# Kernel tuning notes

Hardware: AMD Instinct MI355X
Metric: run time of the kernel (lower is better)

## Reference

```python
import jax, jax.numpy as jnp
import numpy as np

D = 512
H = 8
DH = D // H
EPS = 1e-5


def layer_norm(x, gamma, beta):
    mu = jnp.mean(x, axis=-1, keepdims=True)
    var = jnp.mean(jnp.square(x - mu), axis=-1, keepdims=True)
    return (x - mu) * jax.lax.rsqrt(var + EPS) * gamma + beta


def setup_inputs() -> dict:
    key = jax.random.key(0)
    ks = jax.random.split(key, 16)
    B, N = 16, 1024
    s = 1.0 / np.sqrt(D)
    return {
        "h": jax.random.normal(ks[0], (B, N, D), jnp.float32),
        "ln1_g": jnp.ones((D,), jnp.float32),
        "ln1_b": jnp.zeros((D,), jnp.float32),
        "wq": jax.random.normal(ks[1], (D, D), jnp.float32) * s,
        "bq": jnp.zeros((D,), jnp.float32),
        "wk": jax.random.normal(ks[2], (D, D), jnp.float32) * s,
        "bk": jnp.zeros((D,), jnp.float32),
        "wv": jax.random.normal(ks[3], (D, D), jnp.float32) * s,
        "bv": jnp.zeros((D,), jnp.float32),
        "wo": jax.random.normal(ks[4], (D, D), jnp.float32) * s,
        "bo": jnp.zeros((D,), jnp.float32),
        "ln2_g": jnp.ones((D,), jnp.float32),
        "ln2_b": jnp.zeros((D,), jnp.float32),
        "w1": jax.random.normal(ks[5], (2 * D, D), jnp.float32) * s,
        "b1": jnp.zeros((2 * D,), jnp.float32),
        "w2": jax.random.normal(ks[6], (D, 2 * D), jnp.float32) * (1.0 / np.sqrt(2 * D)),
        "b2": jnp.zeros((D,), jnp.float32),
    }


def reference(h, ln1_g, ln1_b, wq, bq, wk, bk, wv, bv, wo, bo,
              ln2_g, ln2_b, w1, b1, w2, b2):
    B, N, _ = h.shape
    hn = layer_norm(h, ln1_g, ln1_b)
    # projections (torch Linear convention: x @ W^T + b)
    q = (hn @ wq.T + bq).reshape(B, N, H, DH)
    k = (hn @ wk.T + bk).reshape(B, N, H, DH)
    v = (hn @ wv.T + bv).reshape(B, N, H, DH)
    scores = jnp.einsum("bqhd,bkhd->bhqk", q, k) / np.sqrt(DH)
    attn = jax.nn.softmax(scores, axis=-1)  # [B,H,N,N]
    ctx = jnp.einsum("bhqk,bkhd->bqhd", attn, v).reshape(B, N, D)
    attn_out = ctx @ wo.T + bo
    # averaged attention weights (torch default average_attn_weights=True)
    attn_weights = jnp.mean(attn, axis=1)  # [B,N,N]
    h = h + attn_out
    # FFN: LN -> Linear(d,2d) -> SiLU -> Linear(2d,d), residual
    f = layer_norm(h, ln2_g, ln2_b)
    f = jax.nn.silu(f @ w1.T + b1) @ w2.T + b2
    h = h + f
    return h, attn_weights
```

## Files before the change

### kernel.cpp

```cpp
#include <hip/hip_runtime.h>

typedef unsigned short u16;
typedef __attribute__((ext_vector_type(8))) short short8;
typedef __attribute__((ext_vector_type(4))) float floatx4;
typedef __attribute__((ext_vector_type(16))) float floatx16;

#define MFMA_BF16(a, b, c) __builtin_amdgcn_mfma_f32_16x16x32_bf16((a), (b), (c), 0, 0, 0)
#define MFMA32(a, b, c) __builtin_amdgcn_mfma_f32_32x32x16_bf16((a), (b), (c), 0, 0, 0)

__device__ __forceinline__ u16 f2bf(float f) {
  unsigned b = __float_as_uint(f);
  b = b + 0x7FFFu + ((b >> 16) & 1u);
  return (u16)(b >> 16);
}

__device__ __forceinline__ float fexp8(float s) {
  float r;
  asm("v_exp_f32 %0, %1" : "=v"(r) : "v"(s * 0.18033688011112042f));
  return r;
}

__device__ __forceinline__ unsigned cvtpk(float a, float b) {
  unsigned r;
  asm("v_cvt_pk_bf16_f32 %0, %1, %2" : "=v"(r) : "v"(a), "v"(b));
  return r;
}

__device__ __forceinline__ void plswap(unsigned& x, unsigned& y) {
  asm("v_permlane32_swap_b32 %0, %1" : "+v"(x), "+v"(y));
}

__device__ __forceinline__ void gll16(const u16* g, u16* lds_uniform) {
  __builtin_amdgcn_global_load_lds(
      (const __attribute__((address_space(1))) void*)g,
      (__attribute__((address_space(3))) void*)lds_uniform, 16, 0, 0);
}

__global__ __launch_bounds__(256) void cast4_kernel(const float* __restrict__ src,
                                                    u16* __restrict__ dst, int n4) {
  int i = blockIdx.x * 256 + threadIdx.x;
  if (i < n4) {
    float4 v = ((const float4*)src)[i];
    ushort4 o;
    o.x = f2bf(v.x); o.y = f2bf(v.y); o.z = f2bf(v.z); o.w = f2bf(v.w);
    ((ushort4*)dst)[i] = o;
  }
}

__global__ __launch_bounds__(128) void ln_kernel(const float* __restrict__ x,
                                                 const float* __restrict__ g,
                                                 const float* __restrict__ be,
                                                 u16* __restrict__ y) {
  int row = blockIdx.x, t = threadIdx.x;
  float4 v = ((const float4*)(x + (size_t)row * 512))[t];
  float s = v.x + v.y + v.z + v.w;
  float q = v.x * v.x + v.y * v.y + v.z * v.z + v.w * v.w;
#pragma unroll
  for (int off = 32; off > 0; off >>= 1) {
    s += __shfl_xor(s, off);
    q += __shfl_xor(q, off);
  }
  __shared__ float sb[2], qb[2];
  int w = t >> 6;
  if ((t & 63) == 0) { sb[w] = s; qb[w] = q; }
  __syncthreads();
  s = sb[0] + sb[1];
  q = qb[0] + qb[1];
  float mu = s * (1.0f / 512.0f);
  float var = q * (1.0f / 512.0f) - mu * mu;
  float rs = rsqrtf(var + 1e-5f);
  float4 gg = ((const float4*)g)[t];
  float4 bb = ((const float4*)be)[t];
  ushort4 o;
  o.x = f2bf((v.x - mu) * rs * gg.x + bb.x);
  o.y = f2bf((v.y - mu) * rs * gg.y + bb.y);
  o.z = f2bf((v.z - mu) * rs * gg.z + bb.z);
  o.w = f2bf((v.w - mu) * rs * gg.w + bb.w);
  ((ushort4*)(y + (size_t)row * 512))[t] = o;
}

template <bool OUTB, bool SILU, bool RES>
__global__ __launch_bounds__(256) void gemm_bt_kernel(
    const u16* __restrict__ A, const u16* __restrict__ W,
    const float* __restrict__ bias, const float* __restrict__ res,
    void* __restrict__ out, int N, int K) {
  __shared__ __align__(16) u16 As[128 * 32];
  __shared__ __align__(16) u16 Bs[128 * 32];
  int t = threadIdx.x;
  int lane = t & 63, wave = t >> 6;
  int l15 = lane & 15, quad = lane >> 4;
  int rowBlk = blockIdx.y * 128, colBlk = blockIdx.x * 128;
  const u16* Ag = A + (size_t)(rowBlk + (t >> 2)) * K + (t & 3) * 8;
  const u16* Wg = W + (size_t)(colBlk + (t >> 2)) * K + (t & 3) * 8;
  u16* AsW = As + wave * 512;
  u16* BsW = Bs + wave * 512;
  int arow = (wave >> 1) * 64;
  int brow = (wave & 1) * 64;
  floatx4 acc[4][4] = {};
  for (int k0 = 0; k0 < K; k0 += 32) {
    gll16(Ag + k0, AsW);
    gll16(Ag + (size_t)64 * K + k0, AsW + 2048);
    gll16(Wg + k0, BsW);
    gll16(Wg + (size_t)64 * K + k0, BsW + 2048);
    __syncthreads();
    short8 a[4], b[4];
#pragma unroll
    for (int i = 0; i < 4; ++i)
      a[i] = *(const short8*)(As + (size_t)(arow + i * 16 + l15) * 32 + quad * 8);
#pragma unroll
    for (int j = 0; j < 4; ++j)
      b[j] = *(const short8*)(Bs + (size_t)(brow + j * 16 + l15) * 32 + quad * 8);
#pragma unroll
    for (int i = 0; i < 4; ++i)
#pragma unroll
      for (int j = 0; j < 4; ++j)
        acc[i][j] = MFMA_BF16(a[i], b[j], acc[i][j]);
    __syncthreads();
  }
#pragma unroll
  for (int j = 0; j < 4; ++j) {
    int col = colBlk + brow + j * 16 + l15;
    float bs = bias[col];
#pragma unroll
    for (int i = 0; i < 4; ++i) {
      int row0 = rowBlk + arow + i * 16 + quad * 4;
#pragma unroll
      for (int r = 0; r < 4; ++r) {
        size_t idx = (size_t)(row0 + r) * N + col;
        float v = acc[i][j][r] + bs;
        if (RES) v += res[idx];
        if (SILU) v = v * (1.0f / (1.0f + __expf(-v)));
        if (OUTB) ((u16*)out)[idx] = f2bf(v);
        else ((float*)out)[idx] = v;
      }
    }
  }
}

__global__ __launch_bounds__(256) void vtrans_kernel(const u16* __restrict__ qkv,
                                                     u16* __restrict__ vT) {
  __shared__ u16 tile[64][68];
  int blk = blockIdx.x;
  int b = blk >> 7, h = (blk >> 4) & 7, n0 = (blk & 15) * 64;
  int t = threadIdx.x;
#pragma unroll
  for (int rep = 0; rep < 16; ++rep) {
    int idx = t + rep * 256;
    int nl = idx >> 6, dh = idx & 63;
    tile[nl][dh] = qkv[(size_t)(b * 1024 + n0 + nl) * 1536 + 1024 + h * 64 + dh];
  }
  __syncthreads();
#pragma unroll
  for (int rep = 0; rep < 16; ++rep) {
    int idx = t + rep * 256;
    int dh = idx >> 6, nl = idx & 63;
    vT[((size_t)(b * 8 + h) * 64 + dh) * 1024 + n0 + nl] = tile[nl][dh];
  }
}

__global__ __launch_bounds__(256, 4) void attn_ctx_kernel(const u16* __restrict__ qkv,
                                                          const u16* __restrict__ vT,
                                                          u16* __restrict__ ctx,
                                                          float* __restrict__ linv_g) {
  __shared__ __align__(16) u16 Kb[2][4096];
  __shared__ __align__(16) u16 Vb[2][4096];
  int t = threadIdx.x, lane = t & 63, wave = t >> 6;
  int l31 = lane & 31, hi = lane >> 5;
  int bid = blockIdx.x;
  int L = (bid & 7) * 128 + (bid >> 3);
  int qblk = L & 7, h = (L >> 3) & 7, b = L >> 6;
  int q0w = qblk * 128 + wave * 32;

  short8 qf[4];
  const u16* qbase = qkv + (size_t)(b * 1024 + q0w + l31) * 1536 + h * 64;
#pragma unroll
  for (int t4 = 0; t4 < 4; ++t4)
    qf[t4] = *(const short8*)(qbase + t4 * 16 + hi * 8);

  short8 ones;
#pragma unroll
  for (int i = 0; i < 8; ++i) ones[i] = (short)0x3F80;

  floatx16 oacc[2] = {};
  floatx16 psum = {};

  const u16* krow = qkv + (size_t)(b * 1024 + lane) * 1536 + 512 + h * 64;
  const u16* vrow = vT + ((size_t)(b * 8 + h) * 64 + lane) * 1024;

  gll16(krow + wave * 8, &Kb[0][wave * 512]);
  gll16(krow + (wave + 4) * 8, &Kb[0][(wave + 4) * 512]);
  gll16(vrow + wave * 8, &Vb[0][wave * 512]);
  gll16(vrow + (wave + 4) * 8, &Vb[0][(wave + 4) * 512]);
  __syncthreads();

#pragma unroll 1
  for (int c = 0; c < 16; ++c) {
    int bf = c & 1;
    if (c < 15) {
      int nc = (c + 1) * 64;
      gll16(krow + (size_t)nc * 1536 + wave * 8, &Kb[bf ^ 1][wave * 512]);
      gll16(krow + (size_t)nc * 1536 + (wave + 4) * 8, &Kb[bf ^ 1][(wave + 4) * 512]);
      gll16(vrow + nc + wave * 8, &Vb[bf ^ 1][wave * 512]);
      gll16(vrow + nc + (wave + 4) * 8, &Vb[bf ^ 1][(wave + 4) * 512]);
    }
    short8 pa[4];
#pragma unroll
    for (int ct = 0; ct < 2; ++ct) {
      floatx16 s = {};
#pragma unroll
      for (int t4 = 0; t4 < 4; ++t4) {
        short8 kf = *(const short8*)&Kb[bf][(t4 * 2 + hi) * 512 + (ct * 32 + l31) * 8];
        s = MFMA32(kf, qf[t4], s);
      }
#pragma unroll
      for (int r = 0; r < 16; ++r) s[r] = fexp8(s[r]);
#pragma unroll
      for (int j = 0; j < 2; ++j) {
        unsigned a0 = cvtpk(s[j * 8 + 0], s[j * 8 + 1]);
        unsigned b0 = cvtpk(s[j * 8 + 4], s[j * 8 + 5]);
        unsigned a1 = cvtpk(s[j * 8 + 2], s[j * 8 + 3]);
        unsigned b1 = cvtpk(s[j * 8 + 6], s[j * 8 + 7]);
        plswap(a0, b0);
        plswap(a1, b1);
        union { unsigned u[4]; short8 v8; } uu;
        uu.u[0] = a0; uu.u[1] = a1; uu.u[2] = b0; uu.u[3] = b1;
        pa[ct * 2 + j] = uu.v8;
      }
    }
#pragma unroll
    for (int ks = 0; ks < 4; ++ks) {
      psum = MFMA32(pa[ks], ones, psum);
#pragma unroll
      for (int ct2 = 0; ct2 < 2; ++ct2) {
        short8 vf = *(const short8*)&Vb[bf][(ks * 2 + hi) * 512 + (ct2 * 32 + l31) * 8];
        oacc[ct2] = MFMA32(pa[ks], vf, oacc[ct2]);
      }
    }
    __syncthreads();
  }

  float il[16];
#pragma unroll
  for (int r = 0; r < 16; ++r) il[r] = 1.0f / psum[r];
  if (l31 == 0) {
#pragma unroll
    for (int reg = 0; reg < 16; ++reg) {
      int row = (reg & 3) + 8 * (reg >> 2) + 4 * hi;
      linv_g[(size_t)(b * 8 + h) * 1024 + q0w + row] = il[reg];
    }
  }
#pragma unroll
  for (int ct = 0; ct < 2; ++ct)
#pragma unroll
    for (int reg = 0; reg < 16; ++reg) {
      int row = (reg & 3) + 8 * (reg >> 2) + 4 * hi;
      ctx[(size_t)(b * 1024 + q0w + row) * 512 + h * 64 + ct * 32 + l31] =
          f2bf(oacc[ct][reg] * il[reg]);
    }
}

__global__ __launch_bounds__(256, 2) void attn_avg_kernel(const u16* __restrict__ qkv,
                                                          const float* __restrict__ linv_g,
                                                          float* __restrict__ attnw) {
  __shared__ __align__(16) u16 Ks[8 * 4096];
  int t = threadIdx.x, lane = t & 63, wave = t >> 6;
  int l31 = lane & 31, hi = lane >> 5;
  int bid = blockIdx.x;
  int L = (bid & 7) * 64 + (bid >> 3);
  int b = L >> 5;
  int r5 = L & 31;
  int kq = r5 & 3, qb = r5 >> 2;
  int q0w = qb * 128 + wave * 32;
  int key0 = kq * 256;

  const u16* qbase = qkv + (size_t)(b * 1024 + q0w + l31) * 1536;

  floatx16 avgacc[2] = {};
#pragma unroll 1
  for (int c = 0; c < 4; ++c) {
    const u16* kbase = qkv + (size_t)(b * 1024 + key0 + c * 64 + lane) * 1536 + 512;
#pragma unroll
    for (int s = 0; s < 16; ++s) {
      int idx = wave * 16 + s;
      int hh = idx >> 3, g = idx & 7;
      gll16(kbase + hh * 64 + g * 8, Ks + hh * 4096 + g * 512);
    }
    __syncthreads();
#pragma unroll 2
    for (int h = 0; h < 8; ++h) {
      short8 qf[4];
#pragma unroll
      for (int t4 = 0; t4 < 4; ++t4)
        qf[t4] = *(const short8*)(qbase + h * 64 + t4 * 16 + hi * 8);
      const float* lg = linv_g + (size_t)(b * 8 + h) * 1024 + q0w + 4 * hi;
      float4 il0 = *(const float4*)(lg);
      float4 il1 = *(const float4*)(lg + 8);
      float4 il2 = *(const float4*)(lg + 16);
      float4 il3 = *(const float4*)(lg + 24);
      float il[16] = {il0.x, il0.y, il0.z, il0.w, il1.x, il1.y, il1.z, il1.w,
                      il2.x, il2.y, il2.z, il2.w, il3.x, il3.y, il3.z, il3.w};
#pragma unroll
      for (int ct = 0; ct < 2; ++ct) {
        floatx16 sacc = {};
#pragma unroll
        for (int t4 = 0; t4 < 4; ++t4) {
          short8 kf = *(const short8*)(Ks + h * 4096 + (t4 * 2 + hi) * 512 +
                                       (ct * 32 + l31) * 8);
          sacc = MFMA32(qf[t4], kf, sacc);
        }
#pragma unroll
        for (int r = 0; r < 16; ++r)
          avgacc[ct][r] += fexp8(sacc[r]) * il[r];
      }
    }
    __syncthreads();
    int cb = key0 + c * 64;
#pragma unroll
    for (int ct = 0; ct < 2; ++ct)
#pragma unroll
      for (int r = 0; r < 16; ++r) {
        int row = (r & 3) + 8 * (r >> 2) + 4 * hi;
        __builtin_nontemporal_store(
            avgacc[ct][r] * 0.125f,
            &attnw[(size_t)(b * 1024 + q0w + row) * 1024 + cb + ct * 32 + l31]);
        avgacc[ct][r] = 0.f;
      }
  }
}

extern "C" void kernel_launch(void* const* d_in, const int* in_sizes, int n_in,
                              void* d_out, int out_size, void* d_ws, size_t ws_size,
                              hipStream_t stream) {
  (void)in_sizes; (void)n_in; (void)out_size; (void)ws_size;
  const float* h   = (const float*)d_in[0];
  const float* g1  = (const float*)d_in[1];
  const float* be1 = (const float*)d_in[2];
  const float* wq  = (const float*)d_in[3];
  const float* bq  = (const float*)d_in[4];
  const float* wk  = (const float*)d_in[5];
  const float* bk  = (const float*)d_in[6];
  const float* wv  = (const float*)d_in[7];
  const float* bv  = (const float*)d_in[8];
  const float* wo  = (const float*)d_in[9];
  const float* bo  = (const float*)d_in[10];
  const float* g2  = (const float*)d_in[11];
  const float* be2 = (const float*)d_in[12];
  const float* w1  = (const float*)d_in[13];
  const float* b1  = (const float*)d_in[14];
  const float* w2  = (const float*)d_in[15];
  const float* b2  = (const float*)d_in[16];

  char* p = (char*)d_ws;
  auto carve = [&](size_t bytes) {
    char* r = p;
    p += (bytes + 255) & ~(size_t)255;
    return r;
  };
  u16*   wcat = (u16*)carve((size_t)1536 * 512 * 2);
  u16*   wob  = (u16*)carve((size_t)512 * 512 * 2);
  u16*   w1b  = (u16*)carve((size_t)1024 * 512 * 2);
  u16*   w2b  = (u16*)carve((size_t)512 * 1024 * 2);
  float* bcat = (float*)carve((size_t)1536 * 4);
  u16*   hn   = (u16*)carve((size_t)16384 * 512 * 2);
  u16*   qkvb = (u16*)carve((size_t)16384 * 1536 * 2);
  u16*   vTb  = (u16*)carve((size_t)16384 * 512 * 2);
  u16*   ctxb = (u16*)carve((size_t)16384 * 512 * 2);
  u16*   fb   = (u16*)carve((size_t)16384 * 512 * 2);
  u16*   gb   = (u16*)carve((size_t)16384 * 1024 * 2);
  float* linv = (float*)carve((size_t)16 * 8 * 1024 * 4);

  float* outh = (float*)d_out;
  float* outattn = outh + (size_t)16384 * 512;

  cast4_kernel<<<256, 256, 0, stream>>>(wq, wcat, 65536);
  cast4_kernel<<<256, 256, 0, stream>>>(wk, wcat + 512 * 512, 65536);
  cast4_kernel<<<256, 256, 0, stream>>>(wv, wcat + 2 * 512 * 512, 65536);
  cast4_kernel<<<256, 256, 0, stream>>>(wo, wob, 65536);
  cast4_kernel<<<512, 256, 0, stream>>>(w1, w1b, 131072);
  cast4_kernel<<<512, 256, 0, stream>>>(w2, w2b, 131072);
  hipMemcpyAsync(bcat, bq, 512 * 4, hipMemcpyDeviceToDevice, stream);
  hipMemcpyAsync(bcat + 512, bk, 512 * 4, hipMemcpyDeviceToDevice, stream);
  hipMemcpyAsync(bcat + 1024, bv, 512 * 4, hipMemcpyDeviceToDevice, stream);

  ln_kernel<<<16384, 128, 0, stream>>>(h, g1, be1, hn);
  gemm_bt_kernel<true, false, false><<<dim3(12, 128), 256, 0, stream>>>(
      hn, wcat, bcat, nullptr, qkvb, 1536, 512);
  vtrans_kernel<<<2048, 256, 0, stream>>>(qkvb, vTb);
  attn_ctx_kernel<<<1024, 256, 0, stream>>>(qkvb, vTb, ctxb, linv);
  attn_avg_kernel<<<512, 256, 0, stream>>>(qkvb, linv, outattn);
  gemm_bt_kernel<false, false, true><<<dim3(4, 128), 256, 0, stream>>>(
      ctxb, wob, bo, h, outh, 512, 512);
  ln_kernel<<<16384, 128, 0, stream>>>(outh, g2, be2, fb);
  gemm_bt_kernel<true, true, false><<<dim3(8, 128), 256, 0, stream>>>(
      fb, w1b, b1, nullptr, gb, 1024, 512);
  gemm_bt_kernel<false, false, true><<<dim3(4, 128), 256, 0, stream>>>(
      gb, w2b, b2, outh, outh, 512, 1024);
}
```

Baseline: 438.2 us.

## Restructure attention-average kernel: smaller key tiles, staged swizzled Q/K in LDS

The attention-weight averaging kernel now gives each block 64 keys instead of 256 and launches four times as many blocks. Each block loops over heads and stages both Q and K per head into XOR-swizzled LDS tiles, instead of loading Q from global per head with a large 64KB K buffer. LDS use drops from 64KB to 24KB, and launch bounds rise to 4 blocks per SM to improve occupancy and reduce bank conflicts. In exchange, each Q tile is reloaded by 16 blocks instead of 4, which adds global and L2 traffic, and the kernel now syncs once per head.

```diff
diff --git a/kernel.cpp b/kernel.cpp
--- a/kernel.cpp
+++ b/kernel.cpp
@@ -259,72 +259,88 @@
     }
 }
 
-__global__ __launch_bounds__(256, 2) void attn_avg_kernel(const u16* __restrict__ qkv,
+__global__ __launch_bounds__(256, 4) void attn_avg_kernel(const u16* __restrict__ qkv,
                                                           const float* __restrict__ linv_g,
                                                           float* __restrict__ attnw) {
-  __shared__ __align__(16) u16 Ks[8 * 4096];
+  __shared__ __align__(16) u16 Qs[128 * 64];
+  __shared__ __align__(16) u16 Ks[64 * 64];
   int t = threadIdx.x, lane = t & 63, wave = t >> 6;
   int l31 = lane & 31, hi = lane >> 5;
   int bid = blockIdx.x;
-  int L = (bid & 7) * 64 + (bid >> 3);
-  int b = L >> 5;
-  int r5 = L & 31;
-  int kq = r5 & 3, qb = r5 >> 2;
-  int q0w = qb * 128 + wave * 32;
-  int key0 = kq * 256;
-
-  const u16* qbase = qkv + (size_t)(b * 1024 + q0w + l31) * 1536;
-
-  floatx16 avgacc[2] = {};
+  int L = (bid & 7) * 256 + (bid >> 3);
+  int b = L >> 7;
+  int r7 = L & 127;
+  int kq = r7 & 15, qb = r7 >> 4;
+  int q0 = qb * 128;
+  int q0w = q0 + wave * 32;
+  int key0 = kq * 64;
+
+  int li = lane >> 3, sl = lane & 7;
+
+  floatx16 acc0 = {}, acc1 = {};
+
 #pragma unroll 1
-  for (int c = 0; c < 4; ++c) {
-    const u16* kbase = qkv + (size_t)(b * 1024 + key0 + c * 64 + lane) * 1536 + 512;
-#pragma unroll
-    for (int s = 0; s < 16; ++s) {
-      int idx = wave * 16 + s;
-      int hh = idx >> 3, g = idx & 7;
-      gll16(kbase + hh * 64 + g * 8, Ks + hh * 4096 + g * 512);
+  for (int h = 0; h < 8; ++h) {
+    {
+      const u16* qsec = qkv + (size_t)(b * 1024 + q0) * 1536 + h * 64;
+#pragma unroll
+      for (int j = 0; j < 4; ++j) {
+        int r0 = wave * 32 + j * 8;
+        int row = r0 + li;
+        gll16(qsec + (size_t)row * 1536 + ((sl ^ (row & 7)) << 3), Qs + r0 * 64);
+      }
+      const u16* ksec = qkv + (size_t)(b * 1024 + key0) * 1536 + 512 + h * 64;
+#pragma unroll
+      for (int j = 0; j < 2; ++j) {
+        int r0 = wave * 16 + j * 8;
+        int row = r0 + li;
+        gll16(ksec + (size_t)row * 1536 + ((sl ^ (row & 7)) << 3), Ks + r0 * 64);
+      }
     }
     __syncthreads();
-#pragma unroll 2
-    for (int h = 0; h < 8; ++h) {
-      short8 qf[4];
-#pragma unroll
-      for (int t4 = 0; t4 < 4; ++t4)
-        qf[t4] = *(const short8*)(qbase + h * 64 + t4 * 16 + hi * 8);
-      const float* lg = linv_g + (size_t)(b * 8 + h) * 1024 + q0w + 4 * hi;
-      float4 il0 = *(const float4*)(lg);
-      float4 il1 = *(const float4*)(lg + 8);
-      float4 il2 = *(const float4*)(lg + 16);
-      float4 il3 = *(const float4*)(lg + 24);
-      float il[16] = {il0.x, il0.y, il0.z, il0.w, il1.x, il1.y, il1.z, il1.w,
-                      il2.x, il2.y, il2.z, il2.w, il3.x, il3.y, il3.z, il3.w};
-#pragma unroll
-      for (int ct = 0; ct < 2; ++ct) {
-        floatx16 sacc = {};
-#pragma unroll
-        for (int t4 = 0; t4 < 4; ++t4) {
-          short8 kf = *(const short8*)(Ks + h * 4096 + (t4 * 2 + hi) * 512 +
-                                       (ct * 32 + l31) * 8);
-          sacc = MFMA32(qf[t4], kf, sacc);
-        }
-#pragma unroll
-        for (int r = 0; r < 16; ++r)
-          avgacc[ct][r] += fexp8(sacc[r]) * il[r];
+
+    const float* lg = linv_g + (size_t)(b * 8 + h) * 1024 + q0w + 4 * hi;
+    float4 il0 = *(const float4*)(lg);
+    float4 il1 = *(const float4*)(lg + 8);
+    float4 il2 = *(const float4*)(lg + 16);
+    float4 il3 = *(const float4*)(lg + 24);
+    float il[16] = {il0.x, il0.y, il0.z, il0.w, il1.x, il1.y, il1.z, il1.w,
+                    il2.x, il2.y, il2.z, il2.w, il3.x, il3.y, il3.z, il3.w};
+
+    short8 qf[4];
+#pragma unroll
+    for (int t4 = 0; t4 < 4; ++t4) {
+      int row = wave * 32 + l31;
+      int g2 = t4 * 2 + hi;
+      qf[t4] = *(const short8*)(Qs + row * 64 + ((g2 ^ (row & 7)) << 3));
+    }
+#pragma unroll
+    for (int ct = 0; ct < 2; ++ct) {
+      floatx16 sacc = {};
+#pragma unroll
+      for (int t4 = 0; t4 < 4; ++t4) {
+        int key = ct * 32 + l31;
+        int g2 = t4 * 2 + hi;
+        short8 kf = *(const short8*)(Ks + key * 64 + ((g2 ^ (key & 7)) << 3));
+        sacc = MFMA32(qf[t4], kf, sacc);
+      }
+      if (ct == 0) {
+#pragma unroll
+        for (int r = 0; r < 16; ++r) acc0[r] += fexp8(sacc[r]) * il[r];
+      } else {
+#pragma unroll
+        for (int r = 0; r < 16; ++r) acc1[r] += fexp8(sacc[r]) * il[r];
       }
     }
     __syncthreads();
-    int cb = key0 + c * 64;
-#pragma unroll
-    for (int ct = 0; ct < 2; ++ct)
-#pragma unroll
-      for (int r = 0; r < 16; ++r) {
-        int row = (r & 3) + 8 * (r >> 2) + 4 * hi;
-        __builtin_nontemporal_store(
-            avgacc[ct][r] * 0.125f,
-            &attnw[(size_t)(b * 1024 + q0w + row) * 1024 + cb + ct * 32 + l31]);
-        avgacc[ct][r] = 0.f;
-      }
+  }
+
+#pragma unroll
+  for (int r = 0; r < 16; ++r) {
+    int row = (r & 3) + 8 * (r >> 2) + 4 * hi;
+    float* dst = &attnw[(size_t)(b * 1024 + q0w + row) * 1024 + key0 + l31];
+    __builtin_nontemporal_store(acc0[r] * 0.125f, dst);
+    __builtin_nontemporal_store(acc1[r] * 0.125f, dst + 32);
   }
 }
 
@@ -387,7 +403,7 @@
       hn, wcat, bcat, nullptr, qkvb, 1536, 512);
   vtrans_kernel<<<2048, 256, 0, stream>>>(qkvb, vTb);
   attn_ctx_kernel<<<1024, 256, 0, stream>>>(qkvb, vTb, ctxb, linv);
-  attn_avg_kernel<<<512, 256, 0, stream>>>(qkvb, linv, outattn);
+  attn_avg_kernel<<<2048, 256, 0, stream>>>(qkvb, linv, outattn);
   gemm_bt_kernel<false, false, true><<<dim3(4, 128), 256, 0, stream>>>(
       ctxb, wob, bo, h, outh, 512, 512);
   ln_kernel<<<16384, 128, 0, stream>>>(outh, g2, be2, fb);
```

Result: faster. 416.7 us (-4.9%).
